# Optimization experiments

Measured on AMD Instinct MI355X. Metric: run time of the kernel, lower is better.

## Reference

```python
import jax, jax.numpy as jnp
import numpy as np

N, L, H, E = 4, 2048, 8, 64
S, D = 2048, 64
EPS = 1e-6

def setup_inputs() -> dict:
    key = jax.random.key(0)
    k1, k2, k3 = jax.random.split(key, 3)
    return {
        "queries": jax.random.normal(k1, (N, L, H, E), dtype=jnp.float32),
        "keys": jax.random.normal(k2, (N, S, H, E), dtype=jnp.float32),
        "values": jax.random.normal(k3, (N, S, H, D), dtype=jnp.float32),
        "key_mask": jnp.ones((N, S), dtype=jnp.float32),
    }

def reference(queries, keys, values, key_mask):
    n, l, h, e = queries.shape
    _, s, _, d = values.shape
    softmax_temp = 1.0 / np.sqrt(e).astype(np.float32)
    # Faithful to torch: .view(N,H,L,E) is a reshape of the contiguous
    # (N,L,H,E) buffer, NOT a transpose.
    q = queries.reshape(n, h, l, e)
    k = keys.reshape(n, h, s, e)
    # squared euclidean distance ||q_i - k_j||^2 via expansion (== cdist^2)
    q_sq = jnp.sum(q * q, axis=-1)  # [n,h,l]
    k_sq = jnp.sum(k * k, axis=-1)  # [n,h,s]
    qk = jnp.einsum('nhle,nhse->nhls', q, k)
    dist_sq = jnp.maximum(q_sq[..., :, None] + k_sq[..., None, :] - 2.0 * qk, 0.0)
    phi = jnp.exp(-softmax_temp * (dist_sq * 0.5))  # [n,h,l,s]
    phi = phi * key_mask[:, None, None, :]
    Z = 1.0 / (jnp.sum(phi, axis=-1) + EPS)  # [n,h,l]
    out = jnp.einsum('nhls,nshd,nhl->nlhd', phi, values, Z)
    return out
```

## Files before the change

kernel.cpp:

```cpp
#include <hip/hip_runtime.h>
#include <stdint.h>


#define N_ 4
#define L_ 2048
#define H_ 8
#define S_ 2048

#define C1 0.18033688f
#define C2 0.09016844f

typedef unsigned short ushort_t;
typedef unsigned int uint_t;
typedef __bf16 b8 __attribute__((ext_vector_type(8)));
typedef float f4 __attribute__((ext_vector_type(4)));
typedef const __attribute__((address_space(1))) uint32_t* gas_ptr;
typedef __attribute__((address_space(3))) uint32_t* las_ptr;

static __device__ __forceinline__ ushort_t f2bf(float x) {
  uint32_t u = __float_as_uint(x);
  u += 0x7fffu + ((u >> 16) & 1u);
  return (ushort_t)(u >> 16);
}

__global__ __launch_bounds__(256) void k_prep(const float* __restrict__ ksrc,
                                              ushort_t* __restrict__ kdst,
                                              float* __restrict__ lbf,
                                              const float* __restrict__ mask,
                                              const float* __restrict__ v,
                                              ushort_t* __restrict__ vt) {
  __shared__ __align__(16) ushort_t tile[64][68];
  if (blockIdx.x < 1024) {
    int t = blockIdx.x * 256 + threadIdx.x;
    int row = t >> 2, part = t & 3;
    const float4* p = reinterpret_cast<const float4*>(ksrc + (size_t)row * 64 + part * 16);
    uint_t o[8];
    float s = 0.f;
#pragma unroll
    for (int i = 0; i < 4; ++i) {
      float4 vv = p[i];
      s += vv.x * vv.x + vv.y * vv.y + vv.z * vv.z + vv.w * vv.w;
      o[2 * i]     = (uint_t)f2bf(vv.x) | ((uint_t)f2bf(vv.y) << 16);
      o[2 * i + 1] = (uint_t)f2bf(vv.z) | ((uint_t)f2bf(vv.w) << 16);
    }
    uint4* dp = reinterpret_cast<uint4*>(kdst + (size_t)row * 64 + part * 16);
    dp[0] = make_uint4(o[0], o[1], o[2], o[3]);
    dp[1] = make_uint4(o[4], o[5], o[6], o[7]);
    s += __shfl_xor(s, 1);
    s += __shfl_xor(s, 2);
    if (part == 0) {
      int n = row >> 14;
      int sidx = row & (S_ - 1);
      float m = mask[n * S_ + sidx];
      lbf[row] = -C2 * s + __log2f(m);
    }
  } else {
    const int vb = blockIdx.x - 1024;
    const int sc = vb & 31;
    const int h = (vb >> 5) & 7;
    const int n = vb >> 8;
    const int t = threadIdx.x;
    const int sl = t >> 4;
    const int dp = (t & 15) * 4;
#pragma unroll
    for (int i = 0; i < 4; ++i) {
      int s = sc * 64 + i * 16 + sl;
      float4 val = *reinterpret_cast<const float4*>(
          v + (((size_t)n * S_ + s) * H_ + h) * 64 + dp);
      tile[dp + 0][i * 16 + sl] = f2bf(val.x);
      tile[dp + 1][i * 16 + sl] = f2bf(val.y);
      tile[dp + 2][i * 16 + sl] = f2bf(val.z);
      tile[dp + 3][i * 16 + sl] = f2bf(val.w);
    }
    __syncthreads();
    const int d = t >> 2, sp = (t & 3) * 16;
    uint_t o[8];
#pragma unroll
    for (int i = 0; i < 8; ++i) {
      const int p0 = sp + 2 * i, p1 = p0 + 1;
      const int s0 = (p0 & 32) + (((p0 >> 2) & 1) << 4) + (((p0 >> 3) & 3) << 2) + (p0 & 3);
      const int s1 = (p1 & 32) + (((p1 >> 2) & 1) << 4) + (((p1 >> 3) & 3) << 2) + (p1 & 3);
      o[i] = (uint_t)tile[d][s0] | ((uint_t)tile[d][s1] << 16);
    }
    size_t base = ((size_t)(n * H_ + h) * 64 + d) * S_ + sc * 64 + sp;
    uint4* w = reinterpret_cast<uint4*>(vt + base);
    w[0] = make_uint4(o[0], o[1], o[2], o[3]);
    w[1] = make_uint4(o[4], o[5], o[6], o[7]);
  }
}

__global__ __launch_bounds__(256, 4) void k_attn(
    const float* __restrict__ qf32, const ushort_t* __restrict__ kb,
    const ushort_t* __restrict__ vt, const float* __restrict__ lbf,
    float* __restrict__ out) {
  __shared__ __align__(16) ushort_t kt[2][64 * 64];
  __shared__ __align__(16) ushort_t vtt[2][64 * 64];
  __shared__ __align__(16) float zb[4][16];

  const int lane = threadIdx.x & 63;
  const int w = threadIdx.x >> 6;
  const int bid = blockIdx.x;
  const int swz = (bid & 7) * 128 + (bid >> 3);
  const int qt = swz & 31;
  const int hd = (swz >> 5) & 7;
  const int n = swz >> 8;
  const int nh = n * H_ + hd;
  const int c = lane & 15;
  const int g = lane >> 4;
  const int qrow0 = qt * 64 + w * 16;

  union U4 { uint_t u[4]; b8 v; };

  const float* qsrc = qf32 + ((size_t)nh * L_ + qrow0) * 64;
  b8 qfr[2];
  float epsr;
  {
    const float* rp = qsrc + (size_t)c * 64 + g * 8;
    float s = 0.f;
#pragma unroll
    for (int es = 0; es < 2; ++es) {
      float4 v0 = *reinterpret_cast<const float4*>(rp + es * 32);
      float4 v1 = *reinterpret_cast<const float4*>(rp + es * 32 + 4);
      s += v0.x * v0.x + v0.y * v0.y + v0.z * v0.z + v0.w * v0.w
         + v1.x * v1.x + v1.y * v1.y + v1.z * v1.z + v1.w * v1.w;
      U4 tq;
      tq.u[0] = (uint_t)f2bf(v0.x) | ((uint_t)f2bf(v0.y) << 16);
      tq.u[1] = (uint_t)f2bf(v0.z) | ((uint_t)f2bf(v0.w) << 16);
      tq.u[2] = (uint_t)f2bf(v1.x) | ((uint_t)f2bf(v1.y) << 16);
      tq.u[3] = (uint_t)f2bf(v1.z) | ((uint_t)f2bf(v1.w) << 16);
      qfr[es] = tq.v;
    }
    s += __shfl_xor(s, 16);
    s += __shfl_xor(s, 32);
    epsr = 1e-6f * __builtin_amdgcn_exp2f(C2 * s);
  }

  const ushort_t* kbh = kb + (size_t)nh * S_ * 64;
  const ushort_t* vth = vt + (size_t)nh * 64 * S_;
  const float* lbh = lbf + (size_t)nh * S_;

  f4 zero4 = {0.f, 0.f, 0.f, 0.f};
  f4 acc[4] = {zero4, zero4, zero4, zero4};
  float rs = 0.f;

  const int lrow = lane >> 3;
  const int lc16 = (lane & 7) ^ lrow;

  float4 lbA[4], lbB[4];

#define WAITV8 asm volatile("s_waitcnt vmcnt(8)" ::: "memory")
#define WAITV4 asm volatile("s_waitcnt vmcnt(4)" ::: "memory")

#define STAGE(bufi, ch)                                                        \
  {                                                                            \
    _Pragma("unroll")                                                          \
    for (int t2 = 0; t2 < 2; ++t2) {                                           \
      const int rr = w * 16 + t2 * 8;                                          \
      const ushort_t* gk = kbh + ((size_t)(ch) * 64 + rr + lrow) * 64 + lc16 * 8; \
      __builtin_amdgcn_global_load_lds((gas_ptr)gk, (las_ptr)(&kt[bufi][rr * 64]), 16, 0, 0); \
      const ushort_t* gv = vth + (size_t)(rr + lrow) * S_ + (ch) * 64 + lc16 * 8; \
      __builtin_amdgcn_global_load_lds((gas_ptr)gv, (las_ptr)(&vtt[bufi][rr * 64]), 16, 0, 0); \
    }                                                                          \
  }

#define LBLOAD(dst, ch)                                                        \
  {                                                                            \
    _Pragma("unroll")                                                          \
    for (int ss = 0; ss < 4; ++ss)                                             \
      dst[ss] = *reinterpret_cast<const float4*>(lbh + (ch) * 64 + ss * 16 + 4 * g); \
  }

#define CHUNK(CH, BUF, LBC, LBN, DO_LB, DO_S, WAITX)                           \
  {                                                                            \
    WAITX;                                                                     \
    __builtin_amdgcn_s_barrier();                                              \
    __builtin_amdgcn_sched_barrier(0);                                         \
    uint_t pw[8];                                                              \
    _Pragma("unroll")                                                          \
    for (int ss = 0; ss < 4; ++ss) {                                           \
      const ushort_t* ktb = &kt[BUF][(ss * 16 + c) * 64];                      \
      b8 ak0 = *reinterpret_cast<const b8*>(ktb + (g ^ (c & 7)) * 8);          \
      b8 ak1 = *reinterpret_cast<const b8*>(ktb + ((4 + g) ^ (c & 7)) * 8);    \
      __builtin_amdgcn_s_setprio(1);                                           \
      f4 s0 = __builtin_amdgcn_mfma_f32_16x16x32_bf16(ak0, qfr[0], zero4, 0, 0, 0); \
      s0 = __builtin_amdgcn_mfma_f32_16x16x32_bf16(ak1, qfr[1], s0, 0, 0, 0);  \
      __builtin_amdgcn_s_setprio(0);                                           \
      float p0 = __builtin_amdgcn_exp2f(fmaf(C1, s0[0], LBC[ss].x));           \
      float p1 = __builtin_amdgcn_exp2f(fmaf(C1, s0[1], LBC[ss].y));           \
      float p2 = __builtin_amdgcn_exp2f(fmaf(C1, s0[2], LBC[ss].z));           \
      float p3 = __builtin_amdgcn_exp2f(fmaf(C1, s0[3], LBC[ss].w));           \
      rs += (p0 + p1) + (p2 + p3);                                             \
      asm("v_cvt_pk_bf16_f32 %0, %1, %2" : "=v"(pw[2 * ss])     : "v"(p0), "v"(p1)); \
      asm("v_cvt_pk_bf16_f32 %0, %1, %2" : "=v"(pw[2 * ss + 1]) : "v"(p2), "v"(p3)); \
    }                                                                          \
    __builtin_amdgcn_s_setprio(1);                                             \
    _Pragma("unroll")                                                          \
    for (int sst = 0; sst < 2; ++sst) {                                        \
      U4 pa;                                                                   \
      pa.u[0] = pw[4 * sst + 0]; pa.u[1] = pw[4 * sst + 1];                    \
      pa.u[2] = pw[4 * sst + 2]; pa.u[3] = pw[4 * sst + 3];                    \
      _Pragma("unroll")                                                        \
      for (int db = 0; db < 4; ++db) {                                         \
        b8 bv = *reinterpret_cast<const b8*>(                                  \
            &vtt[BUF][(db * 16 + c) * 64] + (((4 * sst + g) ^ (c & 7)) * 8));  \
        acc[db] = __builtin_amdgcn_mfma_f32_16x16x32_bf16(pa.v, bv, acc[db], 0, 0, 0); \
      }                                                                        \
    }                                                                          \
    __builtin_amdgcn_s_setprio(0);                                             \
    __builtin_amdgcn_sched_barrier(0);                                         \
    __builtin_amdgcn_s_barrier();                                              \
    if (DO_LB) { LBLOAD(LBN, (CH) + 1); }                                      \
    __builtin_amdgcn_sched_barrier(0);                                         \
    if (DO_S) { STAGE(BUF, (CH) + 2); }                                        \
  }

  STAGE(0, 0);
  LBLOAD(lbA, 0);
  __builtin_amdgcn_sched_barrier(0);
  STAGE(1, 1);

  for (int ch = 0; ch < 28; ch += 2) {
    CHUNK(ch,     0, lbA, lbB, true, true, WAITV8);
    CHUNK(ch + 1, 1, lbB, lbA, true, true, WAITV8);
  }
  CHUNK(28, 0, lbA, lbB, true,  true,  WAITV8);
  CHUNK(29, 1, lbB, lbA, true,  true,  WAITV8);
  CHUNK(30, 0, lbA, lbB, true,  false, WAITV8);
  CHUNK(31, 1, lbB, lbA, false, false, WAITV4);

#undef CHUNK
#undef STAGE
#undef LBLOAD
#undef WAITV8
#undef WAITV4

  rs += __shfl_xor(rs, 16);
  rs += __shfl_xor(rs, 32);
  if (g == 0) zb[w][c] = 1.f / (rs + epsr);
  __syncthreads();

  const float4 z4 = *reinterpret_cast<const float4*>(&zb[w][4 * g]);
  const float zz[4] = {z4.x, z4.y, z4.z, z4.w};
  float* ob = out + (((size_t)n * L_ + qrow0 + 4 * g) * H_ + hd) * 64;
#pragma unroll
  for (int db = 0; db < 4; ++db) {
#pragma unroll
    for (int r = 0; r < 4; ++r) {
      ob[(size_t)r * (H_ * 64) + db * 16 + c] = acc[db][r] * zz[r];
    }
  }
}

extern "C" void kernel_launch(void* const* d_in, const int* in_sizes, int n_in,
                              void* d_out, int out_size, void* d_ws, size_t ws_size,
                              hipStream_t stream) {
  const float* q = (const float*)d_in[0];
  const float* k = (const float*)d_in[1];
  const float* v = (const float*)d_in[2];
  const float* mask = (const float*)d_in[3];
  float* out = (float*)d_out;

  char* ws = (char*)d_ws;
  ushort_t* kb = (ushort_t*)ws;
  ushort_t* vt = (ushort_t*)(ws + ((size_t)8 << 20));
  float* lbf = (float*)(ws + ((size_t)16 << 20));

  k_prep<<<dim3(2048), dim3(256), 0, stream>>>(k, kb, lbf, mask, v, vt);
  k_attn<<<dim3(1024), dim3(256), 0, stream>>>(q, kb, vt, lbf, out);
}
```

Baseline: 66.54 us.

## Split key chunks across waves instead of query rows, reduce partials in LDS

Result: slower. 84.88 us (+27.6%).

```diff
diff --git a/kernel.cpp b/kernel.cpp
--- a/kernel.cpp
+++ b/kernel.cpp
@@ -76,12 +76,8 @@
     const int d = t >> 2, sp = (t & 3) * 16;
     uint_t o[8];
 #pragma unroll
-    for (int i = 0; i < 8; ++i) {
-      const int p0 = sp + 2 * i, p1 = p0 + 1;
-      const int s0 = (p0 & 32) + (((p0 >> 2) & 1) << 4) + (((p0 >> 3) & 3) << 2) + (p0 & 3);
-      const int s1 = (p1 & 32) + (((p1 >> 2) & 1) << 4) + (((p1 >> 3) & 3) << 2) + (p1 & 3);
-      o[i] = (uint_t)tile[d][s0] | ((uint_t)tile[d][s1] << 16);
-    }
+    for (int i = 0; i < 8; ++i)
+      o[i] = (uint_t)tile[d][sp + 2 * i] | ((uint_t)tile[d][sp + 2 * i + 1] << 16);
     size_t base = ((size_t)(n * H_ + h) * 64 + d) * S_ + sc * 64 + sp;
     uint4* w = reinterpret_cast<uint4*>(vt + base);
     w[0] = make_uint4(o[0], o[1], o[2], o[3]);
@@ -89,13 +85,14 @@
   }
 }
 
-__global__ __launch_bounds__(256, 4) void k_attn(
+__global__ __launch_bounds__(256, 2) void k_attn(
     const float* __restrict__ qf32, const ushort_t* __restrict__ kb,
     const ushort_t* __restrict__ vt, const float* __restrict__ lbf,
     float* __restrict__ out) {
   __shared__ __align__(16) ushort_t kt[2][64 * 64];
   __shared__ __align__(16) ushort_t vtt[2][64 * 64];
-  __shared__ __align__(16) float zb[4][16];
+  __shared__ __align__(16) float rsx[4][4][16];
+  __shared__ __align__(16) float zbz[4][16];
 
   const int lane = threadIdx.x & 63;
   const int w = threadIdx.x >> 6;
@@ -107,15 +104,16 @@
   const int nh = n * H_ + hd;
   const int c = lane & 15;
   const int g = lane >> 4;
-  const int qrow0 = qt * 64 + w * 16;
+  const int qrow0 = qt * 64;
 
   union U4 { uint_t u[4]; b8 v; };
 
   const float* qsrc = qf32 + ((size_t)nh * L_ + qrow0) * 64;
-  b8 qfr[2];
-  float epsr;
-  {
-    const float* rp = qsrc + (size_t)c * 64 + g * 8;
+  b8 qfr[4][2];
+  float epsr[4];
+#pragma unroll
+  for (int t = 0; t < 4; ++t) {
+    const float* rp = qsrc + (size_t)(t * 16 + c) * 64 + g * 8;
     float s = 0.f;
 #pragma unroll
     for (int es = 0; es < 2; ++es) {
@@ -128,11 +126,11 @@
       tq.u[1] = (uint_t)f2bf(v0.z) | ((uint_t)f2bf(v0.w) << 16);
       tq.u[2] = (uint_t)f2bf(v1.x) | ((uint_t)f2bf(v1.y) << 16);
       tq.u[3] = (uint_t)f2bf(v1.z) | ((uint_t)f2bf(v1.w) << 16);
-      qfr[es] = tq.v;
+      qfr[t][es] = tq.v;
     }
     s += __shfl_xor(s, 16);
     s += __shfl_xor(s, 32);
-    epsr = 1e-6f * __builtin_amdgcn_exp2f(C2 * s);
+    epsr[t] = 1e-6f * __builtin_amdgcn_exp2f(C2 * s);
   }
 
   const ushort_t* kbh = kb + (size_t)nh * S_ * 64;
@@ -140,113 +138,187 @@
   const float* lbh = lbf + (size_t)nh * S_;
 
   f4 zero4 = {0.f, 0.f, 0.f, 0.f};
-  f4 acc[4] = {zero4, zero4, zero4, zero4};
-  float rs = 0.f;
+  f4 acc[4][4];
+#pragma unroll
+  for (int t = 0; t < 4; ++t)
+#pragma unroll
+    for (int dt = 0; dt < 4; ++dt) acc[t][dt] = zero4;
+  float rs[4] = {0.f, 0.f, 0.f, 0.f};
+
+  const ushort_t* kb0 = &kt[0][(w * 16 + c) * 64 + ((g) ^ (c & 7)) * 8];
+  const ushort_t* kb1 = &kt[0][(w * 16 + c) * 64 + ((4 + g) ^ (c & 7)) * 8];
+  const ushort_t* vb0 = &vtt[0][c * 64 + (((2 * w + (g >> 1)) ^ (c & 7)) * 8) + (g & 1) * 4];
 
   const int lrow = lane >> 3;
   const int lc16 = (lane & 7) ^ lrow;
 
-  float4 lbA[4], lbB[4];
-
-#define WAITV8 asm volatile("s_waitcnt vmcnt(8)" ::: "memory")
-#define WAITV4 asm volatile("s_waitcnt vmcnt(4)" ::: "memory")
-
-#define STAGE(bufi, ch)                                                        \
+  float4 lbv;
+
+#define WAITV5 asm volatile("s_waitcnt vmcnt(5)" ::: "memory")
+#define WAITV1 asm volatile("s_waitcnt vmcnt(1)" ::: "memory")
+
+#define STAGE(BOFF, ch)                                                        \
   {                                                                            \
     _Pragma("unroll")                                                          \
     for (int t2 = 0; t2 < 2; ++t2) {                                           \
       const int rr = w * 16 + t2 * 8;                                          \
       const ushort_t* gk = kbh + ((size_t)(ch) * 64 + rr + lrow) * 64 + lc16 * 8; \
-      __builtin_amdgcn_global_load_lds((gas_ptr)gk, (las_ptr)(&kt[bufi][rr * 64]), 16, 0, 0); \
+      __builtin_amdgcn_global_load_lds((gas_ptr)gk, (las_ptr)(&kt[0][rr * 64] + (BOFF)), 16, 0, 0); \
       const ushort_t* gv = vth + (size_t)(rr + lrow) * S_ + (ch) * 64 + lc16 * 8; \
-      __builtin_amdgcn_global_load_lds((gas_ptr)gv, (las_ptr)(&vtt[bufi][rr * 64]), 16, 0, 0); \
+      __builtin_amdgcn_global_load_lds((gas_ptr)gv, (las_ptr)(&vtt[0][rr * 64] + (BOFF)), 16, 0, 0); \
     }                                                                          \
   }
 
-#define LBLOAD(dst, ch)                                                        \
-  {                                                                            \
-    _Pragma("unroll")                                                          \
-    for (int ss = 0; ss < 4; ++ss)                                             \
-      dst[ss] = *reinterpret_cast<const float4*>(lbh + (ch) * 64 + ss * 16 + 4 * g); \
-  }
-
-#define CHUNK(CH, BUF, LBC, LBN, DO_LB, DO_S, WAITX)                           \
+#define CHUNK(CH, BOFF, DO_LB, DO_S, WAITX)                                    \
   {                                                                            \
     WAITX;                                                                     \
     __builtin_amdgcn_s_barrier();                                              \
     __builtin_amdgcn_sched_barrier(0);                                         \
     uint_t pw[8];                                                              \
+    b8 ak0 = *reinterpret_cast<const b8*>(kb0 + (BOFF));                       \
+    b8 ak1 = *reinterpret_cast<const b8*>(kb1 + (BOFF));                       \
     _Pragma("unroll")                                                          \
-    for (int ss = 0; ss < 4; ++ss) {                                           \
-      const ushort_t* ktb = &kt[BUF][(ss * 16 + c) * 64];                      \
-      b8 ak0 = *reinterpret_cast<const b8*>(ktb + (g ^ (c & 7)) * 8);          \
-      b8 ak1 = *reinterpret_cast<const b8*>(ktb + ((4 + g) ^ (c & 7)) * 8);    \
+    for (int t = 0; t < 4; ++t) {                                              \
       __builtin_amdgcn_s_setprio(1);                                           \
-      f4 s0 = __builtin_amdgcn_mfma_f32_16x16x32_bf16(ak0, qfr[0], zero4, 0, 0, 0); \
-      s0 = __builtin_amdgcn_mfma_f32_16x16x32_bf16(ak1, qfr[1], s0, 0, 0, 0);  \
+      f4 s0 = __builtin_amdgcn_mfma_f32_16x16x32_bf16(ak0, qfr[t][0], zero4, 0, 0, 0); \
+      s0 = __builtin_amdgcn_mfma_f32_16x16x32_bf16(ak1, qfr[t][1], s0, 0, 0, 0); \
       __builtin_amdgcn_s_setprio(0);                                           \
-      float p0 = __builtin_amdgcn_exp2f(fmaf(C1, s0[0], LBC[ss].x));           \
-      float p1 = __builtin_amdgcn_exp2f(fmaf(C1, s0[1], LBC[ss].y));           \
-      float p2 = __builtin_amdgcn_exp2f(fmaf(C1, s0[2], LBC[ss].z));           \
-      float p3 = __builtin_amdgcn_exp2f(fmaf(C1, s0[3], LBC[ss].w));           \
-      rs += (p0 + p1) + (p2 + p3);                                             \
-      asm("v_cvt_pk_bf16_f32 %0, %1, %2" : "=v"(pw[2 * ss])     : "v"(p0), "v"(p1)); \
-      asm("v_cvt_pk_bf16_f32 %0, %1, %2" : "=v"(pw[2 * ss + 1]) : "v"(p2), "v"(p3)); \
+      float p0 = __builtin_amdgcn_exp2f(fmaf(C1, s0[0], lbv.x));               \
+      float p1 = __builtin_amdgcn_exp2f(fmaf(C1, s0[1], lbv.y));               \
+      float p2 = __builtin_amdgcn_exp2f(fmaf(C1, s0[2], lbv.z));               \
+      float p3 = __builtin_amdgcn_exp2f(fmaf(C1, s0[3], lbv.w));               \
+      rs[t] += (p0 + p1) + (p2 + p3);                                          \
+      asm("v_cvt_pk_bf16_f32 %0, %1, %2" : "=v"(pw[2 * t])     : "v"(p0), "v"(p1)); \
+      asm("v_cvt_pk_bf16_f32 %0, %1, %2" : "=v"(pw[2 * t + 1]) : "v"(p2), "v"(p3)); \
     }                                                                          \
     __builtin_amdgcn_s_setprio(1);                                             \
     _Pragma("unroll")                                                          \
-    for (int sst = 0; sst < 2; ++sst) {                                        \
-      U4 pa;                                                                   \
-      pa.u[0] = pw[4 * sst + 0]; pa.u[1] = pw[4 * sst + 1];                    \
-      pa.u[2] = pw[4 * sst + 2]; pa.u[3] = pw[4 * sst + 3];                    \
+    for (int dt = 0; dt < 4; ++dt) {                                           \
+      U4 bb;                                                                   \
+      uint2 vl = *reinterpret_cast<const uint2*>(vb0 + dt * 1024 + (BOFF));    \
+      bb.u[0] = vl.x; bb.u[1] = vl.y; bb.u[2] = 0u; bb.u[3] = 0u;              \
       _Pragma("unroll")                                                        \
-      for (int db = 0; db < 4; ++db) {                                         \
-        b8 bv = *reinterpret_cast<const b8*>(                                  \
-            &vtt[BUF][(db * 16 + c) * 64] + (((4 * sst + g) ^ (c & 7)) * 8));  \
-        acc[db] = __builtin_amdgcn_mfma_f32_16x16x32_bf16(pa.v, bv, acc[db], 0, 0, 0); \
+      for (int t = 0; t < 4; ++t) {                                            \
+        U4 pa;                                                                 \
+        pa.u[0] = pw[2 * t]; pa.u[1] = pw[2 * t + 1]; pa.u[2] = 0u; pa.u[3] = 0u; \
+        acc[t][dt] = __builtin_amdgcn_mfma_f32_16x16x32_bf16(pa.v, bb.v, acc[t][dt], 0, 0, 0); \
       }                                                                        \
     }                                                                          \
     __builtin_amdgcn_s_setprio(0);                                             \
     __builtin_amdgcn_sched_barrier(0);                                         \
     __builtin_amdgcn_s_barrier();                                              \
-    if (DO_LB) { LBLOAD(LBN, (CH) + 1); }                                      \
+    if (DO_LB) {                                                               \
+      lbv = *reinterpret_cast<const float4*>(lbh + ((CH) + 1) * 64 + w * 16 + 4 * g); \
+    }                                                                          \
     __builtin_amdgcn_sched_barrier(0);                                         \
-    if (DO_S) { STAGE(BUF, (CH) + 2); }                                        \
+    if (DO_S) { STAGE(BOFF, (CH) + 2); }                                       \
   }
 
   STAGE(0, 0);
-  LBLOAD(lbA, 0);
+  lbv = *reinterpret_cast<const float4*>(lbh + 0 * 64 + w * 16 + 4 * g);
   __builtin_amdgcn_sched_barrier(0);
-  STAGE(1, 1);
-
-  for (int ch = 0; ch < 28; ch += 2) {
-    CHUNK(ch,     0, lbA, lbB, true, true, WAITV8);
-    CHUNK(ch + 1, 1, lbB, lbA, true, true, WAITV8);
-  }
-  CHUNK(28, 0, lbA, lbB, true,  true,  WAITV8);
-  CHUNK(29, 1, lbB, lbA, true,  true,  WAITV8);
-  CHUNK(30, 0, lbA, lbB, true,  false, WAITV8);
-  CHUNK(31, 1, lbB, lbA, false, false, WAITV4);
+  STAGE(4096, 1);
+
+#pragma unroll 1
+  for (int ch = 0; ch < 30; ch += 2) {
+    CHUNK(ch,     0,    true, true, WAITV5);
+    CHUNK(ch + 1, 4096, true, true, WAITV5);
+  }
+  CHUNK(30, 0,    true,  false, WAITV5);
+  CHUNK(31, 4096, false, false, WAITV1);
 
 #undef CHUNK
 #undef STAGE
-#undef LBLOAD
-#undef WAITV8
-#undef WAITV4
-
-  rs += __shfl_xor(rs, 16);
-  rs += __shfl_xor(rs, 32);
-  if (g == 0) zb[w][c] = 1.f / (rs + epsr);
-  __syncthreads();
-
-  const float4 z4 = *reinterpret_cast<const float4*>(&zb[w][4 * g]);
+#undef WAITV5
+#undef WAITV1
+
+#pragma unroll
+  for (int t = 0; t < 4; ++t) {
+    rs[t] += __shfl_xor(rs[t], 16);
+    rs[t] += __shfl_xor(rs[t], 32);
+  }
+  if (g == 0) {
+#pragma unroll
+    for (int t = 0; t < 4; ++t) rsx[w][t][c] = rs[t];
+  }
+  __syncthreads();
+
+  float* R0 = reinterpret_cast<float*>(&kt[0][0]);
+  float* R1 = reinterpret_cast<float*>(&vtt[0][0]);
+  const int xb = lane * 16;
+  const int lx = lane & 3;
+
+#pragma unroll
+  for (int dt = 0; dt < 4; ++dt) {
+    const int sl = ((dt ^ lx) & 3) * 4;
+    *reinterpret_cast<f4*>(R0 + w * 1024 + xb + sl) = acc[0][dt];
+    *reinterpret_cast<f4*>(R1 + w * 1024 + xb + sl) = acc[1][dt];
+  }
+  __syncthreads();
+  if (w == 0) {
+#pragma unroll
+    for (int ww = 1; ww < 4; ++ww)
+#pragma unroll
+      for (int dt = 0; dt < 4; ++dt)
+        acc[0][dt] += *reinterpret_cast<const f4*>(R0 + ww * 1024 + xb + ((dt ^ lx) & 3) * 4);
+  } else if (w == 1) {
+#pragma unroll
+    for (int ww = 0; ww < 4; ++ww) {
+      if (ww == 1) continue;
+#pragma unroll
+      for (int dt = 0; dt < 4; ++dt)
+        acc[1][dt] += *reinterpret_cast<const f4*>(R1 + ww * 1024 + xb + ((dt ^ lx) & 3) * 4);
+    }
+  }
+  __syncthreads();
+#pragma unroll
+  for (int dt = 0; dt < 4; ++dt) {
+    const int sl = ((dt ^ lx) & 3) * 4;
+    *reinterpret_cast<f4*>(R0 + w * 1024 + xb + sl) = acc[2][dt];
+    *reinterpret_cast<f4*>(R1 + w * 1024 + xb + sl) = acc[3][dt];
+  }
+  __syncthreads();
+  if (w == 2) {
+#pragma unroll
+    for (int ww = 0; ww < 4; ++ww) {
+      if (ww == 2) continue;
+#pragma unroll
+      for (int dt = 0; dt < 4; ++dt)
+        acc[2][dt] += *reinterpret_cast<const f4*>(R0 + ww * 1024 + xb + ((dt ^ lx) & 3) * 4);
+    }
+  } else if (w == 3) {
+#pragma unroll
+    for (int ww = 0; ww < 4; ++ww) {
+      if (ww == 3) continue;
+#pragma unroll
+      for (int dt = 0; dt < 4; ++dt)
+        acc[3][dt] += *reinterpret_cast<const f4*>(R1 + ww * 1024 + xb + ((dt ^ lx) & 3) * 4);
+    }
+  }
+
+  f4 fin[4] = {zero4, zero4, zero4, zero4};
+  float epsw = 0.f;
+#pragma unroll
+  for (int t = 0; t < 4; ++t) {
+    if (w == t) {
+      fin[0] = acc[t][0]; fin[1] = acc[t][1];
+      fin[2] = acc[t][2]; fin[3] = acc[t][3];
+      epsw = epsr[t];
+    }
+  }
+
+  float rst = rsx[0][w][c] + rsx[1][w][c] + rsx[2][w][c] + rsx[3][w][c];
+  if (g == 0) zbz[w][c] = 1.f / (rst + epsw);
+  __syncthreads();
+
+  const float4 z4 = *reinterpret_cast<const float4*>(&zbz[w][4 * g]);
   const float zz[4] = {z4.x, z4.y, z4.z, z4.w};
-  float* ob = out + (((size_t)n * L_ + qrow0 + 4 * g) * H_ + hd) * 64;
-#pragma unroll
-  for (int db = 0; db < 4; ++db) {
+  float* ob = out + (((size_t)n * L_ + qrow0 + w * 16 + 4 * g) * H_ + hd) * 64;
+#pragma unroll
+  for (int dt = 0; dt < 4; ++dt) {
 #pragma unroll
     for (int r = 0; r < 4; ++r) {
-      ob[(size_t)r * (H_ * 64) + db * 16 + c] = acc[db][r] * zz[r];
+      ob[(size_t)r * (H_ * 64) + dt * 16 + c] = fin[dt][r] * zz[r];
     }
   }
 }
```
